# Kernel optimization log

Hardware: AMD Instinct MI355X
Metric: run time of the kernel (lower is better)

The kernel has to match this reference:

```python
import jax, jax.numpy as jnp
import numpy as np
from jax import lax

# dims
B, D, N_CAMS, P, N_LABELS, A = 256, 2048, 6, 8192, 4096, 6
M = N_CAMS * P                      # 49152 total proxies in concatenated per-cam bank
BETA, BG_KNN, POS_K, TOP_EXTRA = 0.05, 50, 3, 30


def setup_inputs() -> dict:
    key = jax.random.key(0)
    k = jax.random.split(key, 6)
    features = jax.random.normal(k[0], (B, D), jnp.float32)
    bank = jax.random.normal(k[1], (M, D), jnp.float32)
    bank = bank / jnp.linalg.norm(bank, axis=1, keepdims=True)  # ExemplarMemory keeps rows L2-normalized
    cams = jax.random.randint(k[2], (B,), 0, N_CAMS, jnp.int32)
    # global proxy index must lie inside the sample's camera block (mapped_targets = proxy - cam_offset)
    proxy = cams * P + jax.random.randint(k[3], (B,), 0, P, jnp.int32)
    plabel = jax.random.randint(k[4], (B,), 0, N_LABELS, jnp.int32)
    proxy_label_assoc = jax.random.randint(k[5], (N_LABELS, A), 0, M, jnp.int32)
    return {"features": features, "memory_bank": bank, "plabel": plabel,
            "proxy": proxy, "cams": cams, "proxy_label_assoc": proxy_label_assoc}


def _per_cam_mean_sum(vals, cams):
    # original: loop over unique cams, mean within each cam group, sum over cams
    s = jax.ops.segment_sum(vals, cams, num_segments=N_CAMS)
    c = jax.ops.segment_sum(jnp.ones_like(vals), cams, num_segments=N_CAMS)
    return jnp.sum(jnp.where(c > 0, s / jnp.maximum(c, 1.0), 0.0))


def _forward(features, memory_bank, plabel, proxy, cams, proxy_label_assoc):
    bank = lax.stop_gradient(memory_bank)      # percam_tempV is detached; ExemplarMemory bwd treats bank as const
    sims = features @ bank.T                   # [B, M]
    logits = sims / BETA
    sims_d = lax.stop_gradient(sims)
    rows = jnp.arange(B)

    # --- part 1: per-camera ExemplarMemory logits + cross entropy (softmax restricted to own cam block) ---
    col_cam = jnp.arange(M, dtype=jnp.int32) // P          # camera id of each bank column
    block = col_cam[None, :] == cams[:, None]              # [B, M]
    logp = jax.nn.log_softmax(jnp.where(block, logits, -1e9), axis=1)
    ce = -logp[rows, proxy]
    loss = 0.6 * _per_cam_mean_sum(ce, cams)

    # --- part 2: associate loss (cross-camera associated proxies as positives, top-bg_knn hard negatives) ---
    assoc = proxy_label_assoc[plabel]                      # [B, A] ori_asso_ind
    assoc_logits = jnp.take_along_axis(logits, assoc, axis=1)
    masked = sims_d.at[rows[:, None], assoc].set(-10000.0)
    _, neg_idx = lax.top_k(masked, BG_KNN)                 # [B, 50]
    neg_logits = jnp.take_along_axis(logits, neg_idx, axis=1)
    cat = jnp.concatenate([assoc_logits, neg_logits], axis=1)   # [B, A+50]
    lp2 = jax.nn.log_softmax(cat, axis=1)
    assoc_loss = -jnp.mean(lp2[:, :A], axis=1)             # target = 1/A on associated slots
    loss = loss + 0.7 * _per_cam_mean_sum(assoc_loss, cams)

    # --- part 3: online loss (per-camera argmax tops, top-3 as positives, +30 hard negatives) ---
    cam_arg = jnp.argmax(sims_d.reshape(B, N_CAMS, P), axis=2).astype(jnp.int32)
    cam_tops = cam_arg + (jnp.arange(N_CAMS, dtype=jnp.int32) * P)[None, :]   # [B, N_CAMS] global idx
    cam_top_sims = jnp.take_along_axis(sims_d, cam_tops, axis=1)
    _, sel3 = lax.top_k(cam_top_sims, POS_K)
    pos_idx = jnp.take_along_axis(cam_tops, sel3, axis=1)   # [B, 3]
    boosted = sims_d.at[rows[:, None], pos_idx].set(10000.0)
    _, top_idx = lax.top_k(boosted, TOP_EXTRA + POS_K)      # positives (10000) come first in descending order
    sel_logits = jnp.take_along_axis(logits, top_idx, axis=1)
    lp3 = jax.nn.log_softmax(sel_logits, axis=1)
    online_loss = -jnp.mean(lp3[:, :POS_K], axis=1)         # target = 1/3 on the 3 positives
    loss = loss + 0.7 * _per_cam_mean_sum(online_loss, cams)
    return loss


def reference(features, memory_bank, plabel, proxy, cams, proxy_label_assoc):
    return _forward(features, memory_bank, plabel, proxy, cams, proxy_label_assoc)
```

## Files before the change

kernel.cpp:

```cpp
#include <hip/hip_runtime.h>

#define MDIM 49152
#define BDIM 256
#define DDIM 2048
#define PDIM 8192
#define NCAMS 6
#define INV_BETA 20.0f
#define UFILT 0xBFC00000u

typedef __attribute__((ext_vector_type(8))) short bf16x8;
typedef __attribute__((ext_vector_type(4))) float f32x4;

static __device__ __forceinline__ unsigned short f2bf(float f) {
  unsigned u = __float_as_uint(f);
  unsigned r = 0x7FFFu + ((u >> 16) & 1u);
  return (unsigned short)((u + r) >> 16);
}

static __device__ __forceinline__ unsigned f2u(float f) {
  unsigned u = __float_as_uint(f);
  return (u & 0x80000000u) ? ~u : (u | 0x80000000u);
}
static __device__ __forceinline__ float u2f(unsigned u) {
  return __uint_as_float((u & 0x80000000u) ? (u & 0x7FFFFFFFu) : ~u);
}

static __device__ __forceinline__ void gload_lds16(void* lds, const void* g) {
  __builtin_amdgcn_global_load_lds((const __attribute__((address_space(1))) unsigned int*)g,
                                   (__attribute__((address_space(3))) unsigned int*)lds,
                                   16, 0, 0);
}

__global__ __launch_bounds__(256) void conv_feat(
    const float* __restrict__ feat, unsigned short* __restrict__ fb)
{
  const int i = (blockIdx.x * 256 + threadIdx.x) * 4;
  const float4 v = *(const float4*)(feat + i);
  ushort4 p;
  p.x = f2bf(v.x); p.y = f2bf(v.y); p.z = f2bf(v.z); p.w = f2bf(v.w);
  *(ushort4*)(fb + i) = p;
}

__global__ __launch_bounds__(256) void gemm_kernel(
    const unsigned short* __restrict__ featb, const float* __restrict__ bank,
    float* __restrict__ sims)
{
  __shared__ unsigned short As[256][64];
  __shared__ unsigned short Bs[64][64];

  const int colTile = blockIdx.x * 64;
  const int t = threadIdx.x;
  const int lane = t & 63;
  const int w = t >> 6;
  const int fr = lane & 15;
  const int quad = lane >> 4;
  const int tr = t >> 4;
  const int tkf = (t & 15) * 4;

  const int arow = w * 64 + (lane >> 3);
  const int acol = (lane & 7) * 8;

  f32x4 acc[4][4];
  #pragma unroll
  for (int i = 0; i < 4; ++i)
    #pragma unroll
    for (int j = 0; j < 4; ++j)
      acc[i][j] = (f32x4){0.f, 0.f, 0.f, 0.f};

  for (int kc = 0; kc < DDIM; kc += 64) {
    #pragma unroll
    for (int q = 0; q < 8; ++q) {
      const unsigned short* g = featb + (size_t)(arow + q * 8) * DDIM + kc + acol;
      gload_lds16(&As[w * 64 + q * 8][0], g);
    }
    #pragma unroll
    for (int p = 0; p < 4; ++p) {
      const int r = p * 16 + tr;
      const float4 vb = *(const float4*)(bank + (size_t)(colTile + r) * DDIM + kc + tkf);
      ushort4 pb; pb.x = f2bf(vb.x); pb.y = f2bf(vb.y); pb.z = f2bf(vb.z); pb.w = f2bf(vb.w);
      *(ushort4*)(&Bs[r][tkf]) = pb;
    }
    __syncthreads();
    #pragma unroll
    for (int kk = 0; kk < 64; kk += 32) {
      bf16x8 fa[4], fb[4];
      #pragma unroll
      for (int i = 0; i < 4; ++i)
        fa[i] = *(const bf16x8*)(&As[w * 64 + i * 16 + fr][kk + quad * 8]);
      #pragma unroll
      for (int j = 0; j < 4; ++j)
        fb[j] = *(const bf16x8*)(&Bs[j * 16 + fr][kk + quad * 8]);
      #pragma unroll
      for (int i = 0; i < 4; ++i)
        #pragma unroll
        for (int j = 0; j < 4; ++j)
          acc[i][j] = __builtin_amdgcn_mfma_f32_16x16x32_bf16(fa[i], fb[j], acc[i][j], 0, 0, 0);
    }
    __syncthreads();
  }

  #pragma unroll
  for (int i = 0; i < 4; ++i) {
    const int row0 = w * 64 + i * 16 + quad * 4;
    #pragma unroll
    for (int j = 0; j < 4; ++j) {
      const int col = colTile + j * 16 + fr;
      #pragma unroll
      for (int r = 0; r < 4; ++r)
        sims[(size_t)(row0 + r) * MDIM + col] = acc[i][j][r];
    }
  }
}

static __device__ __forceinline__ float blk_sum1024(float v, float* buf, int t) {
  buf[t] = v; __syncthreads();
  for (int s = 512; s > 0; s >>= 1) {
    if (t < s) buf[t] += buf[t + s];
    __syncthreads();
  }
  const float r = buf[0]; __syncthreads();
  return r;
}

__global__ __launch_bounds__(1024) void row_kernel(
    const float* __restrict__ sims, const int* __restrict__ plabel,
    const int* __restrict__ proxy, const int* __restrict__ cams,
    const int* __restrict__ assoc, float* __restrict__ losses)
{
  __shared__ unsigned hist[4][2048];
  __shared__ unsigned candU[1024];
  __shared__ int candI[1024];
  __shared__ unsigned ubuf[1024];
  __shared__ float rbuf[1024];
  __shared__ unsigned long long camKey[NCAMS];
  __shared__ unsigned scnt;
  __shared__ int selB;
  __shared__ float sPv[3];
  __shared__ int sPi[3];
  __shared__ float sM;

  const int b = blockIdx.x;
  const int t = threadIdx.x;
  const float* row = sims + (size_t)b * MDIM;

  for (int i = t; i < 4 * 2048; i += 1024) ((unsigned*)hist)[i] = 0u;
  if (t < NCAMS) camKey[t] = 0ull;
  if (t == 0) { scnt = 0u; selB = 0; }
  __syncthreads();

  const int copy = t >> 8;
  unsigned cmU[NCAMS] = {0, 0, 0, 0, 0, 0};
  int cmI[NCAMS] = {0, 0, 0, 0, 0, 0};
  #pragma unroll
  for (int it = 0; it < 12; ++it) {
    const int i = t * 4 + it * 4096;
    const float4 v = *(const float4*)(row + i);
    const float vv[4] = {v.x, v.y, v.z, v.w};
    unsigned bu = 0; int bi = i;
    #pragma unroll
    for (int e = 0; e < 4; ++e) {
      const unsigned u = f2u(vv[e]);
      if (u > UFILT) {
        atomicAdd(&hist[copy][u >> 21], 1u);
        if (u > bu) { bu = u; bi = i + e; }
      }
    }
    if (bu) {
      const int c = i >> 13;
      #pragma unroll
      for (int cc = 0; cc < NCAMS; ++cc)
        if (cc == c && bu > cmU[cc]) { cmU[cc] = bu; cmI[cc] = bi; }
    }
  }
  #pragma unroll
  for (int cc = 0; cc < NCAMS; ++cc)
    if (cmU[cc])
      atomicMax(&camKey[cc],
                ((unsigned long long)cmU[cc] << 32) |
                (unsigned long long)(0xFFFFFFFFu - (unsigned)cmI[cc]));
  __syncthreads();

  if (t == 0) {
    unsigned long long k[NCAMS];
    #pragma unroll
    for (int c = 0; c < NCAMS; ++c) k[c] = camKey[c];
    unsigned used = 0;
    for (int r = 0; r < 3; ++r) {
      int best = 0; unsigned long long bv = 0ull;
      for (int c = 0; c < NCAMS; ++c)
        if (!((used >> c) & 1u) && k[c] > bv) { bv = k[c]; best = c; }
      used |= 1u << best;
      sPv[r] = u2f((unsigned)(bv >> 32));
      sPi[r] = (int)(0xFFFFFFFFu - (unsigned)(bv & 0xFFFFFFFFu));
    }
    sM = sPv[0];
  }

  const int b_lo = 2 * t, b_hi = 2 * t + 1;
  const unsigned h_lo = hist[0][b_lo] + hist[1][b_lo] + hist[2][b_lo] + hist[3][b_lo];
  const unsigned h_hi = hist[0][b_hi] + hist[1][b_hi] + hist[2][b_hi] + hist[3][b_hi];
  ubuf[t] = h_lo + h_hi;
  __syncthreads();
  for (int off = 1; off < 1024; off <<= 1) {
    const unsigned a = ubuf[t];
    const unsigned c = (t + off < 1024) ? ubuf[t + off] : 0u;
    __syncthreads();
    ubuf[t] = a + c;
    __syncthreads();
  }
  const unsigned above = (t < 1023) ? ubuf[t + 1] : 0u;
  const unsigned cum_hi = above + h_hi;
  const unsigned cum_lo = cum_hi + h_lo;
  if (cum_lo >= 56u) atomicMax(&selB, (cum_hi >= 56u) ? b_hi : b_lo);
  __syncthreads();
  const unsigned B1 = (unsigned)selB;

  #pragma unroll
  for (int it = 0; it < 12; ++it) {
    const int i = t * 4 + it * 4096;
    const float4 v = *(const float4*)(row + i);
    const float vv[4] = {v.x, v.y, v.z, v.w};
    #pragma unroll
    for (int e = 0; e < 4; ++e) {
      const unsigned u = f2u(vv[e]);
      if ((u >> 21) >= B1) {
        const unsigned pos = atomicAdd(&scnt, 1u);
        if (pos < 1024u) { candU[pos] = u; candI[pos] = i + e; }
      }
    }
  }
  __syncthreads();
  const int C = (int)min(scnt, 1024u);
  const float m = sM;

  int a6[6];
  {
    const int* ar = assoc + (size_t)plabel[b] * 6;
    #pragma unroll
    for (int e = 0; e < 6; ++e) a6[e] = ar[e];
  }
  float s1 = 0.f;
  if (t < C) {
    const unsigned u = candU[t]; const int ii = candI[t];
    bool ex = false;
    #pragma unroll
    for (int e = 0; e < 6; ++e) ex = ex || (ii == a6[e]);
    if (!ex) {
      int rank = 0;
      for (int j = 0; j < C; ++j) {
        const unsigned u2 = candU[j]; const int i2 = candI[j];
        bool ex2 = false;
        #pragma unroll
        for (int e = 0; e < 6; ++e) ex2 = ex2 || (i2 == a6[e]);
        if (!ex2 && (u2 > u || (u2 == u && i2 < ii))) ++rank;
      }
      if (rank < 50) s1 = __expf((u2f(u) - m) * INV_BETA);
    }
  }
  const float S1n = blk_sum1024(s1, rbuf, t);
  if (t == 0) {
    float S = S1n, am = 0.f;
    #pragma unroll
    for (int e = 0; e < 6; ++e) {
      const float va = row[a6[e]];
      S += __expf((va - m) * INV_BETA);
      am += va;
    }
    losses[BDIM + b] = m * INV_BETA + __logf(S) - am * (INV_BETA / 6.0f);
  }

  float s2 = 0.f;
  if (t < C) {
    const unsigned u = candU[t]; const int ii = candI[t];
    const bool ex = (ii == sPi[0]) || (ii == sPi[1]) || (ii == sPi[2]);
    if (!ex) {
      int rank = 0;
      for (int j = 0; j < C; ++j) {
        const unsigned u2 = candU[j]; const int i2 = candI[j];
        const bool ex2 = (i2 == sPi[0]) || (i2 == sPi[1]) || (i2 == sPi[2]);
        if (!ex2 && (u2 > u || (u2 == u && i2 < ii))) ++rank;
      }
      if (rank < 30) s2 = __expf((u2f(u) - m) * INV_BETA);
    }
  }
  const float S2n = blk_sum1024(s2, rbuf, t);
  if (t == 0) {
    const float p0 = sPv[0], p1 = sPv[1], p2 = sPv[2];
    const float S = S2n + 1.0f + __expf((p1 - m) * INV_BETA) + __expf((p2 - m) * INV_BETA);
    losses[2 * BDIM + b] = m * INV_BETA + __logf(S) - (p0 + p1 + p2) * (INV_BETA / 3.0f);
  }

  const int mycam = cams[b];
  const float m0 = u2f((unsigned)(camKey[mycam] >> 32));
  const float* br = row + mycam * PDIM;
  float s0 = 0.f;
  #pragma unroll
  for (int it = 0; it < 2; ++it) {
    const int i = t * 4 + it * 4096;
    const float4 v = *(const float4*)(br + i);
    s0 += __expf((v.x - m0) * INV_BETA) + __expf((v.y - m0) * INV_BETA) +
          __expf((v.z - m0) * INV_BETA) + __expf((v.w - m0) * INV_BETA);
  }
  const float S0 = blk_sum1024(s0, rbuf, t);
  if (t == 0)
    losses[b] = m0 * INV_BETA + __logf(S0) - row[proxy[b]] * INV_BETA;
}

__global__ __launch_bounds__(256) void final_kernel(
    const float* __restrict__ losses, const int* __restrict__ cams,
    float* __restrict__ out)
{
  __shared__ float s0[NCAMS], s1[NCAMS], s2[NCAMS];
  __shared__ int cnt[NCAMS];
  const int t = threadIdx.x;
  if (t < NCAMS) { s0[t] = 0.f; s1[t] = 0.f; s2[t] = 0.f; cnt[t] = 0; }
  __syncthreads();
  const int c = cams[t];
  atomicAdd(&s0[c], losses[t]);
  atomicAdd(&s1[c], losses[BDIM + t]);
  atomicAdd(&s2[c], losses[2 * BDIM + t]);
  atomicAdd(&cnt[c], 1);
  __syncthreads();
  if (t == 0) {
    float L = 0.f;
    for (int i = 0; i < NCAMS; ++i) {
      if (cnt[i] > 0) {
        const float ic = 1.0f / (float)cnt[i];
        L += 0.6f * s0[i] * ic + 0.7f * s1[i] * ic + 0.7f * s2[i] * ic;
      }
    }
    out[0] = L;
  }
}

extern "C" void kernel_launch(void* const* d_in, const int* in_sizes, int n_in,
                              void* d_out, int out_size, void* d_ws, size_t ws_size,
                              hipStream_t stream) {
  const float* feat   = (const float*)d_in[0];
  const float* bank   = (const float*)d_in[1];
  const int*   plabel = (const int*)d_in[2];
  const int*   proxy  = (const int*)d_in[3];
  const int*   cams   = (const int*)d_in[4];
  const int*   assoc  = (const int*)d_in[5];
  float* out = (float*)d_out;

  float* sims   = (float*)d_ws;
  float* losses = sims + (size_t)BDIM * MDIM;
  unsigned short* featb = (unsigned short*)(losses + 3 * BDIM);

  conv_feat<<<dim3((BDIM * DDIM) / 1024), 256, 0, stream>>>(feat, featb);
  gemm_kernel<<<dim3(MDIM / 64), 256, 0, stream>>>(featb, bank, sims);
  row_kernel<<<dim3(BDIM), 1024, 0, stream>>>(sims, plabel, proxy, cams, assoc, losses);
  final_kernel<<<1, 256, 0, stream>>>(losses, cams, out);
}
```

Measured before the change: 668.8 us.

## Use fixed-threshold candidate collection with histogram fallback, prefetch bank tiles in GEMM

The row kernel now collects top candidates in a single pass using a fixed similarity threshold. It falls back to the histogram-plus-rescan path only when the candidate count is too small or overflows, which removes the shared-memory histogram atomics and second pass in the common case. Per-camera max reduction uses wavefront shuffles before the shared atomics, and there is a fallback for cameras with no positive values. The GEMM register-prefetches the next bank fp32 tile so the global loads overlap the MFMA work. The fixed threshold is tuned to the input distribution, so inputs that miss its range pay for an extra pass.

```diff
diff --git a/kernel.cpp b/kernel.cpp
--- a/kernel.cpp
+++ b/kernel.cpp
@@ -6,7 +6,6 @@
 #define PDIM 8192
 #define NCAMS 6
 #define INV_BETA 20.0f
-#define UFILT 0xBFC00000u
 
 typedef __attribute__((ext_vector_type(8))) short bf16x8;
 typedef __attribute__((ext_vector_type(4))) float f32x4;
@@ -67,20 +66,29 @@
     for (int j = 0; j < 4; ++j)
       acc[i][j] = (f32x4){0.f, 0.f, 0.f, 0.f};
 
+  float4 vb[4];
+  #pragma unroll
+  for (int p = 0; p < 4; ++p)
+    vb[p] = *(const float4*)(bank + (size_t)(colTile + p * 16 + tr) * DDIM + tkf);
+
   for (int kc = 0; kc < DDIM; kc += 64) {
     #pragma unroll
-    for (int q = 0; q < 8; ++q) {
-      const unsigned short* g = featb + (size_t)(arow + q * 8) * DDIM + kc + acol;
-      gload_lds16(&As[w * 64 + q * 8][0], g);
-    }
+    for (int q = 0; q < 8; ++q)
+      gload_lds16(&As[w * 64 + q * 8][0],
+                  featb + (size_t)(arow + q * 8) * DDIM + kc + acol);
     #pragma unroll
     for (int p = 0; p < 4; ++p) {
-      const int r = p * 16 + tr;
-      const float4 vb = *(const float4*)(bank + (size_t)(colTile + r) * DDIM + kc + tkf);
-      ushort4 pb; pb.x = f2bf(vb.x); pb.y = f2bf(vb.y); pb.z = f2bf(vb.z); pb.w = f2bf(vb.w);
-      *(ushort4*)(&Bs[r][tkf]) = pb;
-    }
-    __syncthreads();
+      ushort4 pb;
+      pb.x = f2bf(vb[p].x); pb.y = f2bf(vb[p].y);
+      pb.z = f2bf(vb[p].z); pb.w = f2bf(vb[p].w);
+      *(ushort4*)(&Bs[p * 16 + tr][tkf]) = pb;
+    }
+    __syncthreads();
+    if (kc + 64 < DDIM) {
+      #pragma unroll
+      for (int p = 0; p < 4; ++p)
+        vb[p] = *(const float4*)(bank + (size_t)(colTile + p * 16 + tr) * DDIM + kc + 64 + tkf);
+    }
     #pragma unroll
     for (int kk = 0; kk < 64; kk += 32) {
       bf16x8 fa[4], fb[4];
@@ -137,18 +145,18 @@
   __shared__ int selB;
   __shared__ float sPv[3];
   __shared__ int sPi[3];
-  __shared__ float sM;
 
   const int b = blockIdx.x;
   const int t = threadIdx.x;
   const float* row = sims + (size_t)b * MDIM;
 
-  for (int i = t; i < 4 * 2048; i += 1024) ((unsigned*)hist)[i] = 0u;
   if (t < NCAMS) camKey[t] = 0ull;
   if (t == 0) { scnt = 0u; selB = 0; }
   __syncthreads();
 
-  const int copy = t >> 8;
+  const unsigned UC = f2u(2.75f);
+  const unsigned UPOS = 0x80000000u;
+
   unsigned cmU[NCAMS] = {0, 0, 0, 0, 0, 0};
   int cmI[NCAMS] = {0, 0, 0, 0, 0, 0};
   #pragma unroll
@@ -160,10 +168,11 @@
     #pragma unroll
     for (int e = 0; e < 4; ++e) {
       const unsigned u = f2u(vv[e]);
-      if (u > UFILT) {
-        atomicAdd(&hist[copy][u >> 21], 1u);
-        if (u > bu) { bu = u; bi = i + e; }
-      }
+      if (u >= UC) {
+        const unsigned pos = atomicAdd(&scnt, 1u);
+        if (pos < 1024u) { candU[pos] = u; candI[pos] = i + e; }
+      }
+      if (u > UPOS && u > bu) { bu = u; bi = i + e; }
     }
     if (bu) {
       const int c = i >> 13;
@@ -173,11 +182,16 @@
     }
   }
   #pragma unroll
-  for (int cc = 0; cc < NCAMS; ++cc)
-    if (cmU[cc])
-      atomicMax(&camKey[cc],
-                ((unsigned long long)cmU[cc] << 32) |
-                (unsigned long long)(0xFFFFFFFFu - (unsigned)cmI[cc]));
+  for (int cc = 0; cc < NCAMS; ++cc) {
+    unsigned long long k = ((unsigned long long)cmU[cc] << 32) |
+                           (unsigned long long)(0xFFFFFFFFu - (unsigned)cmI[cc]);
+    #pragma unroll
+    for (int off = 32; off; off >>= 1) {
+      const unsigned long long o = __shfl_down(k, off, 64);
+      if (o > k) k = o;
+    }
+    if ((t & 63) == 0 && (k >> 32)) atomicMax(&camKey[cc], k);
+  }
   __syncthreads();
 
   if (t == 0) {
@@ -193,45 +207,61 @@
       sPv[r] = u2f((unsigned)(bv >> 32));
       sPi[r] = (int)(0xFFFFFFFFu - (unsigned)(bv & 0xFFFFFFFFu));
     }
-    sM = sPv[0];
-  }
-
-  const int b_lo = 2 * t, b_hi = 2 * t + 1;
-  const unsigned h_lo = hist[0][b_lo] + hist[1][b_lo] + hist[2][b_lo] + hist[3][b_lo];
-  const unsigned h_hi = hist[0][b_hi] + hist[1][b_hi] + hist[2][b_hi] + hist[3][b_hi];
-  ubuf[t] = h_lo + h_hi;
-  __syncthreads();
-  for (int off = 1; off < 1024; off <<= 1) {
-    const unsigned a = ubuf[t];
-    const unsigned c = (t + off < 1024) ? ubuf[t + off] : 0u;
-    __syncthreads();
-    ubuf[t] = a + c;
-    __syncthreads();
-  }
-  const unsigned above = (t < 1023) ? ubuf[t + 1] : 0u;
-  const unsigned cum_hi = above + h_hi;
-  const unsigned cum_lo = cum_hi + h_lo;
-  if (cum_lo >= 56u) atomicMax(&selB, (cum_hi >= 56u) ? b_hi : b_lo);
-  __syncthreads();
-  const unsigned B1 = (unsigned)selB;
-
-  #pragma unroll
-  for (int it = 0; it < 12; ++it) {
-    const int i = t * 4 + it * 4096;
-    const float4 v = *(const float4*)(row + i);
-    const float vv[4] = {v.x, v.y, v.z, v.w};
-    #pragma unroll
-    for (int e = 0; e < 4; ++e) {
-      const unsigned u = f2u(vv[e]);
-      if ((u >> 21) >= B1) {
-        const unsigned pos = atomicAdd(&scnt, 1u);
-        if (pos < 1024u) { candU[pos] = u; candI[pos] = i + e; }
-      }
-    }
-  }
-  __syncthreads();
+  }
+  __syncthreads();
+
+  if (scnt < 65u || scnt > 1024u) {
+    for (int i = t; i < 4 * 2048; i += 1024) ((unsigned*)hist)[i] = 0u;
+    __syncthreads();
+    const int copy = t >> 8;
+    #pragma unroll
+    for (int it = 0; it < 12; ++it) {
+      const int i = t * 4 + it * 4096;
+      const float4 v = *(const float4*)(row + i);
+      const float vv[4] = {v.x, v.y, v.z, v.w};
+      #pragma unroll
+      for (int e = 0; e < 4; ++e)
+        atomicAdd(&hist[copy][f2u(vv[e]) >> 21], 1u);
+    }
+    __syncthreads();
+    const int b_lo = 2 * t, b_hi = 2 * t + 1;
+    const unsigned h_lo = hist[0][b_lo] + hist[1][b_lo] + hist[2][b_lo] + hist[3][b_lo];
+    const unsigned h_hi = hist[0][b_hi] + hist[1][b_hi] + hist[2][b_hi] + hist[3][b_hi];
+    ubuf[t] = h_lo + h_hi;
+    __syncthreads();
+    for (int off = 1; off < 1024; off <<= 1) {
+      const unsigned a = ubuf[t];
+      const unsigned c = (t + off < 1024) ? ubuf[t + off] : 0u;
+      __syncthreads();
+      ubuf[t] = a + c;
+      __syncthreads();
+    }
+    const unsigned above = (t < 1023) ? ubuf[t + 1] : 0u;
+    const unsigned cum_hi = above + h_hi;
+    const unsigned cum_lo = cum_hi + h_lo;
+    if (cum_lo >= 56u) atomicMax(&selB, (cum_hi >= 56u) ? b_hi : b_lo);
+    if (t == 0) scnt = 0u;
+    __syncthreads();
+    const unsigned B1 = (unsigned)selB;
+    #pragma unroll
+    for (int it = 0; it < 12; ++it) {
+      const int i = t * 4 + it * 4096;
+      const float4 v = *(const float4*)(row + i);
+      const float vv[4] = {v.x, v.y, v.z, v.w};
+      #pragma unroll
+      for (int e = 0; e < 4; ++e) {
+        const unsigned u = f2u(vv[e]);
+        if ((u >> 21) >= B1) {
+          const unsigned pos = atomicAdd(&scnt, 1u);
+          if (pos < 1024u) { candU[pos] = u; candI[pos] = i + e; }
+        }
+      }
+    }
+    __syncthreads();
+  }
+
   const int C = (int)min(scnt, 1024u);
-  const float m = sM;
+  const float m = sPv[0];
 
   int a6[6];
   {
@@ -291,7 +321,20 @@
   }
 
   const int mycam = cams[b];
-  const float m0 = u2f((unsigned)(camKey[mycam] >> 32));
+  float m0;
+  if (camKey[mycam] != 0ull) {
+    m0 = u2f((unsigned)(camKey[mycam] >> 32));
+  } else {
+    float lm = -3.4e38f;
+    const float* br = row + mycam * PDIM;
+    for (int i = t; i < PDIM; i += 1024) lm = fmaxf(lm, br[i]);
+    rbuf[t] = lm; __syncthreads();
+    for (int s = 512; s > 0; s >>= 1) {
+      if (t < s) rbuf[t] = fmaxf(rbuf[t], rbuf[t + s]);
+      __syncthreads();
+    }
+    m0 = rbuf[0]; __syncthreads();
+  }
   const float* br = row + mycam * PDIM;
   float s0 = 0.f;
   #pragma unroll
```

After: 590.8 us. -11.7%, faster.
